# Kernel optimization log

Hardware: AMD Instinct MI355X
Metric: run time of the kernel (lower is better)

The kernel has to match this reference:

```python
import jax, jax.numpy as jnp
import numpy as np

N_NODES = 10000
N_EDGES = 160000
F_DIM = 64
H = 4


def setup_inputs() -> dict:
    key = jax.random.key(0)
    ks = jax.random.split(key, 10)
    s = 1.0 / np.sqrt(F_DIM)  # xavier-ish scale
    return {
        "x": jax.random.normal(ks[0], (N_NODES, F_DIM), jnp.float32),
        "edge_index": jax.random.randint(ks[1], (2, N_EDGES), 0, N_NODES),
        "edge_vec": jax.random.normal(ks[2], (N_EDGES, 3), jnp.float32),
        "edge_len": jax.random.uniform(ks[3], (N_EDGES,), jnp.float32, 0.1, 5.0),
        "w_proj_W": jax.random.normal(ks[4], (H, F_DIM, F_DIM), jnp.float32) * s,
        "radial_W": jax.random.normal(ks[5], (H, F_DIM, F_DIM), jnp.float32) * s,
        "tangential_W": jax.random.normal(ks[6], (H, F_DIM, F_DIM), jnp.float32) * s,
        "radial_score": jax.random.normal(ks[7], (H, F_DIM), jnp.float32) * s,
        "tangential_score": jax.random.normal(ks[8], (H, F_DIM), jnp.float32) * s,
        "radial_distance_log_scale": jnp.zeros((), jnp.float32),
        "radial_temp_bias": jnp.zeros((H,), jnp.float32),
        "radial_temp_weight": jnp.zeros((H,), jnp.float32),
        "w_out_W": jax.random.normal(ks[9], (F_DIM, F_DIM), jnp.float32) * s,
    }


def _segment_softmax(logits, receiver, num_nodes):
    # logits: [E, H]; softmax over all edges sharing the same receiver.
    # Equivalent to the original's degree-bucketed per-group softmax.
    m = jax.ops.segment_max(logits, receiver, num_segments=num_nodes)  # [N, H]
    a = jnp.exp(logits - m[receiver])
    d = jax.ops.segment_sum(a, receiver, num_segments=num_nodes)       # [N, H]
    return a / d[receiver]


def reference(x, edge_index, edge_vec, edge_len, w_proj_W, radial_W, tangential_W,
              radial_score, tangential_score, radial_distance_log_scale,
              radial_temp_bias, radial_temp_weight, w_out_W):
    sender, receiver = edge_index[0], edge_index[1]
    n = x.shape[0]

    # Per-head bias-free linear projections (o3.Linear on scalar irreps).
    energy = jnp.einsum('nf,hfg->hng', x, w_proj_W)       # [H, N, F]
    radial = jnp.einsum('nf,hfg->hng', x, radial_W)       # [H, N, F]
    tang = jnp.einsum('nf,hfg->hng', x, tangential_W)     # [H, N, F]

    e_d = energy[:, sender] - energy[:, receiver]                       # [H, E, F]
    r_d = jnp.transpose(radial[:, sender] - radial[:, receiver], (1, 0, 2))  # [E, H, F]
    t_d = jnp.transpose(tang[:, sender] - tang[:, receiver], (1, 0, 2))      # [E, H, F]

    scale = jax.nn.softplus(radial_distance_log_scale)
    r_log = jnp.einsum('hef,hf->eh', e_d, radial_score) - scale * edge_len[:, None]  # [E, H]
    temp = jax.nn.softplus(radial_temp_bias[None, :] + radial_temp_weight[None, :] * edge_len[:, None])
    r_log = r_log / (temp + 0.0001)
    t_log = jnp.einsum('hef,hf->eh', e_d, tangential_score)                          # [E, H]

    r_alpha = _segment_softmax(r_log, receiver, n)  # [E, H]
    t_alpha = _segment_softmax(t_log, receiver, n)  # [E, H]

    r_msg = jax.ops.segment_sum(r_alpha[:, :, None] * r_d, receiver, num_segments=n)  # [N, H, F]
    t_msg = jax.ops.segment_sum(t_alpha[:, :, None] * t_d, receiver, num_segments=n)  # [N, H, F]

    out = jnp.nan_to_num((r_msg + t_msg).mean(axis=1))  # mean over heads -> [N, F]
    return x + out @ w_out_W
```

## Files before the change

kernel.cpp:

```cpp
#include <hip/hip_runtime.h>
#include <math.h>

#define N_NODES 10000
#define N_EDGES 160000
#define CAP 64

#define NB_SCORE 40
#define NB_BUCKET 625
#define NB_WPP 9
#define NB_D1 (NB_SCORE + NB_BUCKET + NB_WPP)

typedef short bf16x8 __attribute__((ext_vector_type(8)));
typedef float f32x4 __attribute__((ext_vector_type(4)));

__device__ int g_cur[N_NODES];

__device__ __forceinline__ float bf2f(unsigned short u) {
    return __uint_as_float(((unsigned int)u) << 16);
}
__device__ __forceinline__ unsigned short f2bf(float f) {
    unsigned int x = __float_as_uint(f);
    unsigned int r = (x + 0x7fffu + ((x >> 16) & 1u)) >> 16;
    return (unsigned short)r;
}
__device__ __forceinline__ float softplus_f(float x) {
    return fmaxf(x, 0.f) + log1pf(__expf(-fabsf(x)));
}

__global__ void __launch_bounds__(256) k_prep(const float* __restrict__ x,
                                              const float* __restrict__ wproj,
                                              const float* __restrict__ wrad,
                                              const float* __restrict__ wtan,
                                              const float* __restrict__ rsc,
                                              const float* __restrict__ tsc,
                                              const float* __restrict__ wout,
                                              const int* __restrict__ ei,
                                              const float* __restrict__ el,
                                              float* __restrict__ rts,
                                              int2* __restrict__ sbuf,
                                              unsigned short* __restrict__ wppT) {
    __shared__ __align__(16) float smem[8192];
    int b = blockIdx.x;
    int t = threadIdx.x;

    if (b < NB_SCORE) {
        float* vrl = smem;
        float* vtl = smem + 256;
        {
            int h = t >> 6, f = t & 63;
            const float* wrow = wproj + h * 4096 + f * 64;
            const float* rsp = rsc + h * 64;
            const float* tsp = tsc + h * 64;
            float ar = 0.f, at = 0.f;
            for (int g = 0; g < 64; ++g) {
                float w = wrow[g];
                ar += w * rsp[g];
                at += w * tsp[g];
            }
            vrl[t] = ar;
            vtl[t] = at;
        }
        __syncthreads();
        int n = b * 256 + t;
        if (n >= N_NODES) return;
        const float4* xr = (const float4*)(x + n * 64);
        float accr[4] = {0.f, 0.f, 0.f, 0.f};
        float acct[4] = {0.f, 0.f, 0.f, 0.f};
        for (int i = 0; i < 16; ++i) {
            float4 xv = xr[i];
#pragma unroll
            for (int h = 0; h < 4; ++h) {
                float4 a = ((const float4*)vrl)[h * 16 + i];
                accr[h] += xv.x * a.x + xv.y * a.y + xv.z * a.z + xv.w * a.w;
                float4 bb = ((const float4*)vtl)[h * 16 + i];
                acct[h] += xv.x * bb.x + xv.y * bb.y + xv.z * bb.z + xv.w * bb.w;
            }
        }
        ((float4*)rts)[n * 2]     = make_float4(accr[0], accr[1], accr[2], accr[3]);
        ((float4*)rts)[n * 2 + 1] = make_float4(acct[0], acct[1], acct[2], acct[3]);
    } else if (b < NB_SCORE + NB_BUCKET) {
        int e = (b - NB_SCORE) * 256 + t;
        if (e >= N_EDGES) return;
        int s = ei[e];
        int r = ei[N_EDGES + e];
        float len = el[e];
        int pos = atomicAdd(&g_cur[r], 1);
        if (pos < CAP) sbuf[r * CAP + pos] = make_int2(s, __float_as_int(len));
    } else {
        int k = b - NB_SCORE - NB_BUCKET;
        float* wo = smem;
        float* am = smem + 4096;
        for (int i = 0; i < 16; ++i) wo[t + 256 * i] = wout[t + 256 * i];
        if (k < 8) {
            const float* M = (k < 4) ? (wrad + k * 4096) : (wtan + (k - 4) * 4096);
            for (int i = 0; i < 16; ++i) am[t + 256 * i] = M[t + 256 * i];
        } else {
            for (int i = 0; i < 16; ++i) {
                int e = t + 256 * i;
                float s = 0.f;
#pragma unroll
                for (int h = 0; h < 4; ++h) s += wrad[h * 4096 + e] + wtan[h * 4096 + e];
                am[e] = -s;
            }
        }
        __syncthreads();
        int c = t & 63;
        int fg = t >> 6;
        for (int j = 0; j < 16; ++j) {
            int f = fg * 16 + j;
            float acc = 0.f;
            for (int g = 0; g < 64; ++g) acc += am[f * 64 + g] * wo[g * 64 + c];
            wppT[c * 576 + k * 64 + f] = f2bf(acc * 0.25f);
        }
    }
}

__global__ void __launch_bounds__(512, 8) k_node(const int2* __restrict__ sbuf,
                                                 const float* __restrict__ rts,
                                                 const float* __restrict__ rdls,
                                                 const float* __restrict__ tb,
                                                 const float* __restrict__ tw,
                                                 const float* __restrict__ x,
                                                 const unsigned short* __restrict__ wppT,
                                                 float* __restrict__ out) {
    __shared__ __align__(16) unsigned short accL[16 * 584];
    __shared__ __align__(16) float aldsb[8][CAP * 8];
    __shared__ int sldsb[8][CAP];
    int t = threadIdx.x;
    int wid = t >> 6, lane = t & 63;
    int blk = blockIdx.x;

    float scale = softplus_f(rdls[0]);
    float tb0 = tb[0], tb1 = tb[1], tb2 = tb[2], tb3 = tb[3];
    float tw0 = tw[0], tw1 = tw[1], tw2 = tw[2], tw3 = tw[3];
    float* alds = aldsb[wid];
    int*   slds = sldsb[wid];

    int n = blk * 8 + wid;
    int deg = min(g_cur[n], CAP);
    if (lane == 0) g_cur[n] = 0;

    float4 rsr = ((const float4*)rts)[n * 2];
    float4 tsr = ((const float4*)rts)[n * 2 + 1];

    const float NEG = -3.402823466e38f;
    float rl0 = NEG, rl1 = NEG, rl2 = NEG, rl3 = NEG;
    float tl0 = NEG, tl1 = NEG, tl2 = NEG, tl3 = NEG;
    int s_e = 0;
    if (lane < deg) {
        int2 sl = sbuf[n * CAP + lane];
        s_e = sl.x;
        float len = __int_as_float(sl.y);
        float4 rss = ((const float4*)rts)[s_e * 2];
        float4 tss = ((const float4*)rts)[s_e * 2 + 1];
        float sl0 = scale * len;
        float i0 = 1.f / (softplus_f(tb0 + tw0 * len) + 1e-4f);
        float i1 = 1.f / (softplus_f(tb1 + tw1 * len) + 1e-4f);
        float i2 = 1.f / (softplus_f(tb2 + tw2 * len) + 1e-4f);
        float i3 = 1.f / (softplus_f(tb3 + tw3 * len) + 1e-4f);
        rl0 = ((rss.x - rsr.x) - sl0) * i0;
        rl1 = ((rss.y - rsr.y) - sl0) * i1;
        rl2 = ((rss.z - rsr.z) - sl0) * i2;
        rl3 = ((rss.w - rsr.w) - sl0) * i3;
        tl0 = tss.x - tsr.x;
        tl1 = tss.y - tsr.y;
        tl2 = tss.z - tsr.z;
        tl3 = tss.w - tsr.w;
    }
    float mr0 = rl0, mr1 = rl1, mr2 = rl2, mr3 = rl3;
    float mt0 = tl0, mt1 = tl1, mt2 = tl2, mt3 = tl3;
#pragma unroll
    for (int d = 32; d >= 1; d >>= 1) {
        mr0 = fmaxf(mr0, __shfl_xor(mr0, d)); mr1 = fmaxf(mr1, __shfl_xor(mr1, d));
        mr2 = fmaxf(mr2, __shfl_xor(mr2, d)); mr3 = fmaxf(mr3, __shfl_xor(mr3, d));
        mt0 = fmaxf(mt0, __shfl_xor(mt0, d)); mt1 = fmaxf(mt1, __shfl_xor(mt1, d));
        mt2 = fmaxf(mt2, __shfl_xor(mt2, d)); mt3 = fmaxf(mt3, __shfl_xor(mt3, d));
    }
    float er0 = 0.f, er1 = 0.f, er2 = 0.f, er3 = 0.f;
    float et0 = 0.f, et1 = 0.f, et2 = 0.f, et3 = 0.f;
    if (lane < deg) {
        er0 = __expf(rl0 - mr0); er1 = __expf(rl1 - mr1);
        er2 = __expf(rl2 - mr2); er3 = __expf(rl3 - mr3);
        et0 = __expf(tl0 - mt0); et1 = __expf(tl1 - mt1);
        et2 = __expf(tl2 - mt2); et3 = __expf(tl3 - mt3);
    }
    float sr0 = er0, sr1 = er1, sr2 = er2, sr3 = er3;
    float st0 = et0, st1 = et1, st2 = et2, st3 = et3;
#pragma unroll
    for (int d = 32; d >= 1; d >>= 1) {
        sr0 += __shfl_xor(sr0, d); sr1 += __shfl_xor(sr1, d);
        sr2 += __shfl_xor(sr2, d); sr3 += __shfl_xor(sr3, d);
        st0 += __shfl_xor(st0, d); st1 += __shfl_xor(st1, d);
        st2 += __shfl_xor(st2, d); st3 += __shfl_xor(st3, d);
    }
    if (lane < deg) {
        float* ap = alds + lane * 8;
        ((float4*)ap)[0] = make_float4(er0 / sr0, er1 / sr1, er2 / sr2, er3 / sr3);
        ((float4*)ap)[1] = make_float4(et0 / st0, et1 / st1, et2 / st2, et3 / st3);
        slds[lane] = s_e;
    }

    float a0 = 0.f, a1 = 0.f, a2 = 0.f, a3 = 0.f;
    float b0 = 0.f, b1 = 0.f, b2 = 0.f, b3 = 0.f;
    int i = 0;
    for (; i + 4 <= deg; i += 4) {
        int s0 = slds[i], s1 = slds[i + 1], s2 = slds[i + 2], s3 = slds[i + 3];
        float xv0 = x[s0 * 64 + lane];
        float xv1 = x[s1 * 64 + lane];
        float xv2 = x[s2 * 64 + lane];
        float xv3 = x[s3 * 64 + lane];
        float4 ar0 = ((const float4*)(alds + i * 8))[0];
        float4 at0 = ((const float4*)(alds + i * 8))[1];
        float4 ar1 = ((const float4*)(alds + (i + 1) * 8))[0];
        float4 at1 = ((const float4*)(alds + (i + 1) * 8))[1];
        float4 ar2 = ((const float4*)(alds + (i + 2) * 8))[0];
        float4 at2 = ((const float4*)(alds + (i + 2) * 8))[1];
        float4 ar3 = ((const float4*)(alds + (i + 3) * 8))[0];
        float4 at3 = ((const float4*)(alds + (i + 3) * 8))[1];
        a0 += ar0.x * xv0 + ar1.x * xv1 + ar2.x * xv2 + ar3.x * xv3;
        a1 += ar0.y * xv0 + ar1.y * xv1 + ar2.y * xv2 + ar3.y * xv3;
        a2 += ar0.z * xv0 + ar1.z * xv1 + ar2.z * xv2 + ar3.z * xv3;
        a3 += ar0.w * xv0 + ar1.w * xv1 + ar2.w * xv2 + ar3.w * xv3;
        b0 += at0.x * xv0 + at1.x * xv1 + at2.x * xv2 + at3.x * xv3;
        b1 += at0.y * xv0 + at1.y * xv1 + at2.y * xv2 + at3.y * xv3;
        b2 += at0.z * xv0 + at1.z * xv1 + at2.z * xv2 + at3.z * xv3;
        b3 += at0.w * xv0 + at1.w * xv1 + at2.w * xv2 + at3.w * xv3;
    }
    for (; i < deg; ++i) {
        int s0 = slds[i];
        float xv0 = x[s0 * 64 + lane];
        float4 ar0 = ((const float4*)(alds + i * 8))[0];
        float4 at0 = ((const float4*)(alds + i * 8))[1];
        a0 += ar0.x * xv0; a1 += ar0.y * xv0; a2 += ar0.z * xv0; a3 += ar0.w * xv0;
        b0 += at0.x * xv0; b1 += at0.y * xv0; b2 += at0.z * xv0; b3 += at0.w * xv0;
    }
    float c8 = (deg > 0) ? x[n * 64 + lane] : 0.f;

    unsigned short* arow = accL + wid * 584;
    arow[0 * 64 + lane] = f2bf(a0);
    arow[1 * 64 + lane] = f2bf(a1);
    arow[2 * 64 + lane] = f2bf(a2);
    arow[3 * 64 + lane] = f2bf(a3);
    arow[4 * 64 + lane] = f2bf(b0);
    arow[5 * 64 + lane] = f2bf(b1);
    arow[6 * 64 + lane] = f2bf(b2);
    arow[7 * 64 + lane] = f2bf(b3);
    arow[8 * 64 + lane] = f2bf(c8);
    __syncthreads();

    if (wid < 4) {
        int c = lane & 15, q = lane >> 4;
        f32x4 dacc = {0.f, 0.f, 0.f, 0.f};
        const unsigned short* bp = wppT + (16 * wid + c) * 576 + q * 8;
        const unsigned short* ap = accL + c * 584 + q * 8;
#pragma unroll
        for (int kc = 0; kc < 18; ++kc) {
            bf16x8 af = *(const bf16x8*)(ap + kc * 32);
            bf16x8 bf = *(const bf16x8*)(bp + kc * 32);
            dacc = __builtin_amdgcn_mfma_f32_16x16x32_bf16(af, bf, dacc, 0, 0, 0);
        }
#pragma unroll
        for (int r = 0; r < 4; ++r) {
            int row = q * 4 + r;
            if (row < 8) {
                int node = blk * 8 + row;
                int col = 16 * wid + c;
                out[node * 64 + col] = x[node * 64 + col] + dacc[r];
            }
        }
    }
}

extern "C" void kernel_launch(void* const* d_in, const int* in_sizes, int n_in,
                              void* d_out, int out_size, void* d_ws, size_t ws_size,
                              hipStream_t stream) {
    const float* x     = (const float*)d_in[0];
    const int*   ei    = (const int*)d_in[1];
    const float* el    = (const float*)d_in[3];
    const float* wproj = (const float*)d_in[4];
    const float* wrad  = (const float*)d_in[5];
    const float* wtan  = (const float*)d_in[6];
    const float* rsc   = (const float*)d_in[7];
    const float* tsc   = (const float*)d_in[8];
    const float* rdls  = (const float*)d_in[9];
    const float* tb    = (const float*)d_in[10];
    const float* tw    = (const float*)d_in[11];
    const float* wout  = (const float*)d_in[12];
    float* out = (float*)d_out;

    char* w = (char*)d_ws;
    size_t o = 0;
    auto nxt = [&](size_t bytes) -> char* {
        char* p = w + o;
        o += (bytes + 255) & ~(size_t)255;
        return p;
    };
    float* rts = (float*)nxt((size_t)N_NODES * 8 * 4);
    int2*  sbuf = (int2*)nxt((size_t)N_NODES * CAP * 8);
    unsigned short* wppT = (unsigned short*)nxt((size_t)64 * 576 * 2);

    k_prep<<<NB_D1, 256, 0, stream>>>(x, wproj, wrad, wtan, rsc, tsc, wout,
                                      ei, el, rts, sbuf, wppT);
    k_node<<<1250, 512, 0, stream>>>(sbuf, rts, rdls, tb, tw, x, wppT, out);
}
```

Before: 123.2 us.

## Vectorize edge bucketing, score and weight prep loops; use fast reciprocals

Edge bucketing now processes four edges per thread using int4/float4 loads, cutting the bucket block count to a quarter. The score-vector dot products are vectorized with float4 loads, and the weight-product inner loop is unrolled with four partial accumulators. Divisions in the softmax temperature and normalization are replaced with hardware approximate reciprocals. These changes aim to reduce instruction count and memory transactions in the prep and node kernels, at the cost of slightly less precise division and fewer threads issuing atomics.

```diff
diff --git a/kernel.cpp b/kernel.cpp
--- a/kernel.cpp
+++ b/kernel.cpp
@@ -6,7 +6,7 @@
 #define CAP 64
 
 #define NB_SCORE 40
-#define NB_BUCKET 625
+#define NB_BUCKET 157
 #define NB_WPP 9
 #define NB_D1 (NB_SCORE + NB_BUCKET + NB_WPP)
 
@@ -15,9 +15,6 @@
 
 __device__ int g_cur[N_NODES];
 
-__device__ __forceinline__ float bf2f(unsigned short u) {
-    return __uint_as_float(((unsigned int)u) << 16);
-}
 __device__ __forceinline__ unsigned short f2bf(float f) {
     unsigned int x = __float_as_uint(f);
     unsigned int r = (x + 0x7fffu + ((x >> 16) & 1u)) >> 16;
@@ -48,14 +45,17 @@
         float* vtl = smem + 256;
         {
             int h = t >> 6, f = t & 63;
-            const float* wrow = wproj + h * 4096 + f * 64;
-            const float* rsp = rsc + h * 64;
-            const float* tsp = tsc + h * 64;
+            const float4* wv = (const float4*)(wproj + h * 4096 + f * 64);
+            const float4* rv = (const float4*)(rsc + h * 64);
+            const float4* tv = (const float4*)(tsc + h * 64);
             float ar = 0.f, at = 0.f;
-            for (int g = 0; g < 64; ++g) {
-                float w = wrow[g];
-                ar += w * rsp[g];
-                at += w * tsp[g];
+#pragma unroll
+            for (int g = 0; g < 16; ++g) {
+                float4 w = wv[g];
+                float4 r = rv[g];
+                float4 s2 = tv[g];
+                ar += w.x * r.x + w.y * r.y + w.z * r.z + w.w * r.w;
+                at += w.x * s2.x + w.y * s2.y + w.z * s2.z + w.w * s2.w;
             }
             vrl[t] = ar;
             vtl[t] = at;
@@ -79,13 +79,19 @@
         ((float4*)rts)[n * 2]     = make_float4(accr[0], accr[1], accr[2], accr[3]);
         ((float4*)rts)[n * 2 + 1] = make_float4(acct[0], acct[1], acct[2], acct[3]);
     } else if (b < NB_SCORE + NB_BUCKET) {
-        int e = (b - NB_SCORE) * 256 + t;
-        if (e >= N_EDGES) return;
-        int s = ei[e];
-        int r = ei[N_EDGES + e];
-        float len = el[e];
-        int pos = atomicAdd(&g_cur[r], 1);
-        if (pos < CAP) sbuf[r * CAP + pos] = make_int2(s, __float_as_int(len));
+        int q = (b - NB_SCORE) * 256 + t;
+        if (q * 4 >= N_EDGES) return;
+        int4   sv = ((const int4*)ei)[q];
+        int4   rv = ((const int4*)(ei + N_EDGES))[q];
+        float4 lv = ((const float4*)el)[q];
+        int p0 = atomicAdd(&g_cur[rv.x], 1);
+        if (p0 < CAP) sbuf[rv.x * CAP + p0] = make_int2(sv.x, __float_as_int(lv.x));
+        int p1 = atomicAdd(&g_cur[rv.y], 1);
+        if (p1 < CAP) sbuf[rv.y * CAP + p1] = make_int2(sv.y, __float_as_int(lv.y));
+        int p2 = atomicAdd(&g_cur[rv.z], 1);
+        if (p2 < CAP) sbuf[rv.z * CAP + p2] = make_int2(sv.z, __float_as_int(lv.z));
+        int p3 = atomicAdd(&g_cur[rv.w], 1);
+        if (p3 < CAP) sbuf[rv.w * CAP + p3] = make_int2(sv.w, __float_as_int(lv.w));
     } else {
         int k = b - NB_SCORE - NB_BUCKET;
         float* wo = smem;
@@ -108,9 +114,15 @@
         int fg = t >> 6;
         for (int j = 0; j < 16; ++j) {
             int f = fg * 16 + j;
-            float acc = 0.f;
-            for (int g = 0; g < 64; ++g) acc += am[f * 64 + g] * wo[g * 64 + c];
-            wppT[c * 576 + k * 64 + f] = f2bf(acc * 0.25f);
+            float a0 = 0.f, a1 = 0.f, a2 = 0.f, a3 = 0.f;
+#pragma unroll
+            for (int g = 0; g < 64; g += 4) {
+                a0 += am[f * 64 + g]     * wo[g * 64 + c];
+                a1 += am[f * 64 + g + 1] * wo[(g + 1) * 64 + c];
+                a2 += am[f * 64 + g + 2] * wo[(g + 2) * 64 + c];
+                a3 += am[f * 64 + g + 3] * wo[(g + 3) * 64 + c];
+            }
+            wppT[c * 576 + k * 64 + f] = f2bf(((a0 + a1) + (a2 + a3)) * 0.25f);
         }
     }
 }
@@ -154,10 +166,10 @@
         float4 rss = ((const float4*)rts)[s_e * 2];
         float4 tss = ((const float4*)rts)[s_e * 2 + 1];
         float sl0 = scale * len;
-        float i0 = 1.f / (softplus_f(tb0 + tw0 * len) + 1e-4f);
-        float i1 = 1.f / (softplus_f(tb1 + tw1 * len) + 1e-4f);
-        float i2 = 1.f / (softplus_f(tb2 + tw2 * len) + 1e-4f);
-        float i3 = 1.f / (softplus_f(tb3 + tw3 * len) + 1e-4f);
+        float i0 = __builtin_amdgcn_rcpf(softplus_f(tb0 + tw0 * len) + 1e-4f);
+        float i1 = __builtin_amdgcn_rcpf(softplus_f(tb1 + tw1 * len) + 1e-4f);
+        float i2 = __builtin_amdgcn_rcpf(softplus_f(tb2 + tw2 * len) + 1e-4f);
+        float i3 = __builtin_amdgcn_rcpf(softplus_f(tb3 + tw3 * len) + 1e-4f);
         rl0 = ((rss.x - rsr.x) - sl0) * i0;
         rl1 = ((rss.y - rsr.y) - sl0) * i1;
         rl2 = ((rss.z - rsr.z) - sl0) * i2;
@@ -194,9 +206,13 @@
         st2 += __shfl_xor(st2, d); st3 += __shfl_xor(st3, d);
     }
     if (lane < deg) {
+        float isr0 = __builtin_amdgcn_rcpf(sr0), isr1 = __builtin_amdgcn_rcpf(sr1);
+        float isr2 = __builtin_amdgcn_rcpf(sr2), isr3 = __builtin_amdgcn_rcpf(sr3);
+        float ist0 = __builtin_amdgcn_rcpf(st0), ist1 = __builtin_amdgcn_rcpf(st1);
+        float ist2 = __builtin_amdgcn_rcpf(st2), ist3 = __builtin_amdgcn_rcpf(st3);
         float* ap = alds + lane * 8;
-        ((float4*)ap)[0] = make_float4(er0 / sr0, er1 / sr1, er2 / sr2, er3 / sr3);
-        ((float4*)ap)[1] = make_float4(et0 / st0, et1 / st1, et2 / st2, et3 / st3);
+        ((float4*)ap)[0] = make_float4(er0 * isr0, er1 * isr1, er2 * isr2, er3 * isr3);
+        ((float4*)ap)[1] = make_float4(et0 * ist0, et1 * ist1, et2 * ist2, et3 * ist3);
         slds[lane] = s_e;
     }
 
```

Result: faster. 118.8 us (-3.6%).
